# Optimization experiments

Measured on AMD Instinct MI355X. Metric: run time of the kernel, lower is better.

The kernel has to match this reference:

```python
import jax, jax.numpy as jnp
import numpy as np

N = 100000      # nodes
E = 1600000     # edges
IN = 128        # in_channels
ED = 32         # edge_dim
H = 4           # heads
C = 32          # out_channels per head
NEG_SLOPE = 0.2


def setup_inputs() -> dict:
    key = jax.random.key(0)
    ks = jax.random.split(key, 10)
    s = 0.1  # glorot-ish scale
    return {
        "x": jax.random.normal(ks[0], (N, IN), dtype=jnp.float32),
        "edge_index": jax.random.randint(ks[1], (2, E), 0, N, dtype=jnp.int32),
        "edge_attr": jax.random.normal(ks[2], (E, ED), dtype=jnp.float32),
        "W": jax.random.normal(ks[3], (IN, H * C), dtype=jnp.float32) * s,
        "att_src": jax.random.normal(ks[4], (H, C), dtype=jnp.float32) * s,
        "att_dst": jax.random.normal(ks[5], (H, C), dtype=jnp.float32) * s,
        "W_edge": jax.random.normal(ks[6], (ED, H * C), dtype=jnp.float32) * s,
        "att_edge": jax.random.normal(ks[7], (H, C), dtype=jnp.float32) * s,
        "gat_bias": jnp.zeros((H * C,), dtype=jnp.float32),
        "bias": jnp.zeros((C,), dtype=jnp.float32),
    }


def reference(x, edge_index, edge_attr, W, att_src, att_dst, W_edge, att_edge, gat_bias, bias):
    # eval mode: no dropout. GATConv with edge_dim, concat=True, then mean over heads.
    src, dst = edge_index[0], edge_index[1]
    xh = (x @ W).reshape(N, H, C)                       # [N,H,C]
    a_src = jnp.einsum("nhc,hc->nh", xh, att_src)      # [N,H]
    a_dst = jnp.einsum("nhc,hc->nh", xh, att_dst)      # [N,H]
    eh = (edge_attr @ W_edge).reshape(E, H, C)          # [E,H,C]
    a_edge = jnp.einsum("ehc,hc->eh", eh, att_edge)    # [E,H]
    logits = a_src[src] + a_dst[dst] + a_edge           # [E,H]
    logits = jnp.where(logits >= 0, logits, NEG_SLOPE * logits)  # leaky_relu
    # segment softmax over edges grouped by destination node
    seg_max = jax.ops.segment_max(logits, dst, num_segments=N)  # [N,H]
    expv = jnp.exp(logits - seg_max[dst])
    denom = jax.ops.segment_sum(expv, dst, num_segments=N)      # [N,H]
    alpha = expv / denom[dst]                                    # [E,H]
    msg = xh[src] * alpha[:, :, None]                            # [E,H,C]
    out = jax.ops.segment_sum(msg, dst, num_segments=N)          # [N,H,C]
    out = out + gat_bias.reshape(1, H, C)                        # GATConv bias (concat)
    out = out.mean(axis=1)                                       # combine='mean' -> [N,C]
    out = out + bias
    return jax.nn.relu(out)
```

## Files before the change

### kernel.cpp

```cpp
#include <hip/hip_runtime.h>
#include <hip/hip_bf16.h>

typedef __hip_bfloat16 bf16;

#define N_NODES 100000
#define N_EDGES 1600000
#define IN_CH   128
#define ED_DIM  32
#define HEADS   4
#define C_OUT   32
#define HC      128
#define NEG_SLOPE 0.2f
#define SCAN_BLOCKS 98
#define BP_SLICES 8
#define BP_SLICE_N 12500
#define BP_CHUNKS 6250
#define PREP_BLOCKS 392

__device__ __forceinline__ float bf_lo(unsigned u) { return __uint_as_float(u << 16); }
__device__ __forceinline__ float bf_hi(unsigned u) { return __uint_as_float(u & 0xffff0000u); }
__device__ __forceinline__ unsigned short f2bf_rne(float f) {
    unsigned u = __float_as_uint(f);
    return (unsigned short)((u + 0x7fffu + ((u >> 16) & 1u)) >> 16);
}
__device__ __forceinline__ unsigned pack_bf2(float a, float b) {
    return ((unsigned)f2bf_rne(b) << 16) | f2bf_rne(a);
}
__device__ __forceinline__ float load_any(const void* p, int i, int isf32) {
    return isf32 ? ((const float*)p)[i]
                 : __uint_as_float(((unsigned)((const unsigned short*)p)[i]) << 16);
}

__global__ void report_err(unsigned short* out, float code) {
    if (threadIdx.x < 16) out[threadIdx.x] = f2bf_rne(code);
}

__global__ __launch_bounds__(256) void prep_small(
    const void* __restrict__ x,
    const void* __restrict__ W, const void* __restrict__ att_src,
    const void* __restrict__ att_dst, const void* __restrict__ W_edge,
    const void* __restrict__ att_edge, const void* __restrict__ gat_bias,
    const void* __restrict__ bias,
    int* __restrict__ flag,
    unsigned short* __restrict__ Wc, float* __restrict__ att_src_f,
    float* __restrict__ att_dst_f, float* __restrict__ gat_bias_f,
    float* __restrict__ bias_f, float* __restrict__ Wa,
    int* __restrict__ count) {

    int t = threadIdx.x;
    int gi = blockIdx.x * 256 + t;
    if (gi < N_NODES) count[gi] = 0;
    if (blockIdx.x != 0) return;

    __shared__ int cnt;
    if (t == 0) cnt = 0;
    __syncthreads();
    unsigned xw = ((const unsigned*)x)[t];
    int ex = (xw >> 7) & 0xFF;
    if (ex >= 140) atomicAdd(&cnt, 1);
    __syncthreads();
    int isf32 = (cnt >= 32) ? 1 : 0;
    if (t == 0) *flag = isf32;

    for (int i = t; i < IN_CH * HC; i += 256)
        Wc[i] = f2bf_rne(load_any(W, i, isf32));
    if (t < 128) {
        att_src_f[t]  = load_any(att_src, t, isf32);
        att_dst_f[t]  = load_any(att_dst, t, isf32);
        gat_bias_f[t] = load_any(gat_bias, t, isf32);
    }
    if (t < 32) bias_f[t] = load_any(bias, t, isf32);
    if (t < 128) {
        int d = t & 31, h = t >> 5;
        float acc = 0.f;
        for (int c = 0; c < C_OUT; ++c)
            acc += load_any(W_edge, d * HC + h * C_OUT + c, isf32) *
                   load_any(att_edge, h * C_OUT + c, isf32);
        Wa[h * 32 + d] = acc;
    }
}

__global__ __launch_bounds__(256) void node_gemm(
    const int* __restrict__ flag, const void* __restrict__ x,
    const unsigned short* __restrict__ Wc,
    const float* __restrict__ att_src_f, const float* __restrict__ att_dst_f,
    unsigned short* __restrict__ xh,
    float* __restrict__ a_src, float* __restrict__ a_dst) {

    __shared__ unsigned short Wl[IN_CH * HC];
    __shared__ float xl[32 * IN_CH];

    int isf32 = *flag;
    int t = threadIdx.x;
    int node0 = blockIdx.x * 32;

    const uint4* Wg = (const uint4*)Wc;
    uint4* Wl4 = (uint4*)Wl;
#pragma unroll
    for (int k = 0; k < 8; ++k) Wl4[t + k * 256] = Wg[t + k * 256];

    if (isf32) {
        const float4* xg = (const float4*)((const float*)x + (size_t)node0 * IN_CH);
        float4* xl4 = (float4*)xl;
#pragma unroll
        for (int k = 0; k < 4; ++k) xl4[t + k * 256] = xg[t + k * 256];
    } else {
        const unsigned* xg = (const unsigned*)((const unsigned short*)x + (size_t)node0 * IN_CH);
#pragma unroll
        for (int k = 0; k < 8; ++k) {
            unsigned u = xg[t + k * 256];
            int f = 2 * (t + k * 256);
            xl[f]     = bf_lo(u);
            xl[f + 1] = bf_hi(u);
        }
    }
    __syncthreads();

    int q  = t & 31;
    int i0 = (t >> 5) * 4;
    int j4 = q * 4;
    float acc[16];
#pragma unroll
    for (int k = 0; k < 16; ++k) acc[k] = 0.f;

    const float* xr0 = xl + (i0 + 0) * IN_CH;
    const float* xr1 = xl + (i0 + 1) * IN_CH;
    const float* xr2 = xl + (i0 + 2) * IN_CH;
    const float* xr3 = xl + (i0 + 3) * IN_CH;

#pragma unroll 8
    for (int d = 0; d < IN_CH; ++d) {
        uint2 wb = *(const uint2*)(Wl + d * HC + j4);
        float w0 = bf_lo(wb.x), w1 = bf_hi(wb.x);
        float w2 = bf_lo(wb.y), w3 = bf_hi(wb.y);
        float x0 = xr0[d], x1 = xr1[d], x2 = xr2[d], x3 = xr3[d];
        acc[0]  += x0 * w0; acc[1]  += x0 * w1; acc[2]  += x0 * w2; acc[3]  += x0 * w3;
        acc[4]  += x1 * w0; acc[5]  += x1 * w1; acc[6]  += x1 * w2; acc[7]  += x1 * w3;
        acc[8]  += x2 * w0; acc[9]  += x2 * w1; acc[10] += x2 * w2; acc[11] += x2 * w3;
        acc[12] += x3 * w0; acc[13] += x3 * w1; acc[14] += x3 * w2; acc[15] += x3 * w3;
    }

    float4 sa = *(const float4*)(att_src_f + j4);
    float4 da = *(const float4*)(att_dst_f + j4);

#pragma unroll
    for (int k = 0; k < 4; ++k) {
        int node = node0 + i0 + k;
        float a0 = acc[4 * k], a1 = acc[4 * k + 1], a2 = acc[4 * k + 2], a3 = acc[4 * k + 3];
        *(uint2*)(xh + (size_t)node * HC + j4) =
            make_uint2(pack_bf2(a0, a1), pack_bf2(a2, a3));

        float ps = a0 * sa.x + a1 * sa.y + a2 * sa.z + a3 * sa.w;
        float pd = a0 * da.x + a1 * da.y + a2 * da.z + a3 * da.w;
        ps += __shfl_xor(ps, 1); ps += __shfl_xor(ps, 2); ps += __shfl_xor(ps, 4);
        pd += __shfl_xor(pd, 1); pd += __shfl_xor(pd, 2); pd += __shfl_xor(pd, 4);
        if ((q & 7) == 0) {
            int h = q >> 3;
            a_src[node * HEADS + h] = ps;
            a_dst[node * HEADS + h] = pd;
        }
    }
}

__global__ __launch_bounds__(256) void edge_w(
    const int* __restrict__ flag,
    const int* __restrict__ ei, const void* __restrict__ edge_attr,
    const float* __restrict__ a_src, const float* __restrict__ a_dst,
    const float* __restrict__ Wa,
    uint2* __restrict__ w4b, int* __restrict__ count) {

    __shared__ float WaL[128];
    int t = threadIdx.x;
    if (t < 128) WaL[t] = Wa[t];
    __syncthreads();

    int isf32 = *flag;
    int e = blockIdx.x * 256 + t;
    if (e >= N_EDGES) return;
    int s  = ei[e];
    int dn = ei[N_EDGES + e];

    atomicAdd(&count[dn], 1);

    float ae0 = 0.f, ae1 = 0.f, ae2 = 0.f, ae3 = 0.f;
    if (isf32) {
        const float4* ea = (const float4*)((const float*)edge_attr + (size_t)e * ED_DIM);
#pragma unroll
        for (int k = 0; k < 8; ++k) {
            float4 v = ea[k];
            int d = 4 * k;
            ae0 += v.x * WaL[d] + v.y * WaL[d + 1] + v.z * WaL[d + 2] + v.w * WaL[d + 3];
            ae1 += v.x * WaL[32 + d] + v.y * WaL[33 + d] + v.z * WaL[34 + d] + v.w * WaL[35 + d];
            ae2 += v.x * WaL[64 + d] + v.y * WaL[65 + d] + v.z * WaL[66 + d] + v.w * WaL[67 + d];
            ae3 += v.x * WaL[96 + d] + v.y * WaL[97 + d] + v.z * WaL[98 + d] + v.w * WaL[99 + d];
        }
    } else {
        const uint4* ea = (const uint4*)((const unsigned short*)edge_attr + (size_t)e * ED_DIM);
#pragma unroll
        for (int k = 0; k < 4; ++k) {
            uint4 v = ea[k];
            float g0 = bf_lo(v.x), g1 = bf_hi(v.x), g2 = bf_lo(v.y), g3 = bf_hi(v.y);
            float g4 = bf_lo(v.z), g5 = bf_hi(v.z), g6 = bf_lo(v.w), g7 = bf_hi(v.w);
            int d = 8 * k;
            ae0 += g0*WaL[d] + g1*WaL[d+1] + g2*WaL[d+2] + g3*WaL[d+3]
                 + g4*WaL[d+4] + g5*WaL[d+5] + g6*WaL[d+6] + g7*WaL[d+7];
            ae1 += g0*WaL[32+d] + g1*WaL[33+d] + g2*WaL[34+d] + g3*WaL[35+d]
                 + g4*WaL[36+d] + g5*WaL[37+d] + g6*WaL[38+d] + g7*WaL[39+d];
            ae2 += g0*WaL[64+d] + g1*WaL[65+d] + g2*WaL[66+d] + g3*WaL[67+d]
                 + g4*WaL[68+d] + g5*WaL[69+d] + g6*WaL[70+d] + g7*WaL[71+d];
            ae3 += g0*WaL[96+d] + g1*WaL[97+d] + g2*WaL[98+d] + g3*WaL[99+d]
                 + g4*WaL[100+d] + g5*WaL[101+d] + g6*WaL[102+d] + g7*WaL[103+d];
        }
    }

    float4 as = *(const float4*)(a_src + (size_t)s * 4);
    float4 ad = *(const float4*)(a_dst + (size_t)dn * 4);
    float l0 = as.x + ad.x + ae0;
    float l1 = as.y + ad.y + ae1;
    float l2 = as.z + ad.z + ae2;
    float l3 = as.w + ad.w + ae3;
    l0 = (l0 >= 0.f) ? l0 : NEG_SLOPE * l0;
    l1 = (l1 >= 0.f) ? l1 : NEG_SLOPE * l1;
    l2 = (l2 >= 0.f) ? l2 : NEG_SLOPE * l2;
    l3 = (l3 >= 0.f) ? l3 : NEG_SLOPE * l3;
    float w0 = __expf(l0), w1 = __expf(l1), w2 = __expf(l2), w3 = __expf(l3);

    w4b[e] = make_uint2(pack_bf2(w0, w1), pack_bf2(w2, w3));
}

__global__ __launch_bounds__(256) void scan_a(const int* __restrict__ count,
                                              int* __restrict__ starts,
                                              int* __restrict__ blockSums) {
    __shared__ int sd[256];
    int t = threadIdx.x;
    int base = blockIdx.x * 1024 + t * 4;
    int c0 = (base + 0 < N_NODES) ? count[base + 0] : 0;
    int c1 = (base + 1 < N_NODES) ? count[base + 1] : 0;
    int c2 = (base + 2 < N_NODES) ? count[base + 2] : 0;
    int c3 = (base + 3 < N_NODES) ? count[base + 3] : 0;
    int s = c0 + c1 + c2 + c3;
    sd[t] = s;
    __syncthreads();
    for (int off = 1; off < 256; off <<= 1) {
        int v = (t >= off) ? sd[t - off] : 0;
        __syncthreads();
        sd[t] += v;
        __syncthreads();
    }
    int excl = sd[t] - s;
    if (base + 0 < N_NODES) starts[base + 0] = excl;
    if (base + 1 < N_NODES) starts[base + 1] = excl + c0;
    if (base + 2 < N_NODES) starts[base + 2] = excl + c0 + c1;
    if (base + 3 < N_NODES) starts[base + 3] = excl + c0 + c1 + c2;
    if (t == 255) blockSums[blockIdx.x] = sd[255];
}

__global__ __launch_bounds__(128) void scan_b(int* __restrict__ blockSums) {
    __shared__ int sd[128];
    int t = threadIdx.x;
    int v = (t < SCAN_BLOCKS) ? blockSums[t] : 0;
    sd[t] = v;
    __syncthreads();
    for (int off = 1; off < 128; off <<= 1) {
        int u = (t >= off) ? sd[t - off] : 0;
        __syncthreads();
        sd[t] += u;
        __syncthreads();
    }
    if (t < SCAN_BLOCKS) blockSums[t] = sd[t] - v;
}

__global__ __launch_bounds__(256) void scan_c(int* __restrict__ starts,
                                              int* __restrict__ cursor,
                                              const int* __restrict__ blockSums) {
    int off = blockSums[blockIdx.x];
    int base = blockIdx.x * 1024 + threadIdx.x * 4;
#pragma unroll
    for (int k = 0; k < 4; ++k) {
        int idx = base + k;
        if (idx < N_NODES) {
            int v = starts[idx] + off;
            starts[idx] = v;
            cursor[idx] = v;
        }
    }
    if (blockIdx.x == 0 && threadIdx.x == 0) starts[N_NODES] = N_EDGES;
}

__global__ __launch_bounds__(256) void build_perm(
    const int* __restrict__ ei, const uint2* __restrict__ w4b,
    int* __restrict__ cursor, uint4* __restrict__ perm4) {
    int slice = blockIdx.x & 7;
    int e = (blockIdx.x >> 3) * 256 + threadIdx.x;
    if (e >= N_EDGES) return;
    int dn = ei[N_EDGES + e];
    if (dn < slice * BP_SLICE_N || dn >= (slice + 1) * BP_SLICE_N) return;
    int s = ei[e];
    uint2 wv = w4b[e];
    int pos = atomicAdd(&cursor[dn], 1);
    perm4[pos] = make_uint4((unsigned)s, wv.x, wv.y, 0u);
}

__global__ __launch_bounds__(256) void gather(
    const int* __restrict__ flag,
    const int* __restrict__ starts, const uint4* __restrict__ perm4,
    const unsigned short* __restrict__ xh,
    const float* __restrict__ gat_bias_f, const float* __restrict__ bias_f,
    void* __restrict__ out) {

    __shared__ uint4 sR[4][64];

    int t = threadIdx.x;
    int w = t >> 6, lane = t & 63;
    int quarter = lane >> 4;
    int l = lane & 15;
    int h = l >> 2;
    int n = blockIdx.x * 4 + w;
    if (n >= N_NODES) return;
    int isf32 = *flag;

    int st = starts[n], en = starts[n + 1];
    float f0 = 0.f, f1 = 0.f, f2 = 0.f, f3 = 0.f;
    float f4 = 0.f, f5 = 0.f, f6 = 0.f, f7 = 0.f, wsum = 0.f;

    for (int base = st; base < en; base += 64) {
        int cnt = en - base;
        if (cnt > 64) cnt = 64;
        __builtin_amdgcn_wave_barrier();
        if (lane < cnt) sR[w][lane] = perm4[base + lane];
        __builtin_amdgcn_wave_barrier();
#pragma unroll 4
        for (int jj = 0; jj < cnt; jj += 4) {
            int j = jj + quarter;
            int valid = (j < cnt);
            int jc = valid ? j : jj;
            uint4 r = sR[w][jc];
            int s = (int)r.x;
            unsigned hw = (h & 2) ? r.z : r.y;
            float wt = (h & 1) ? bf_hi(hw) : bf_lo(hw);
            wt = valid ? wt : 0.f;
            uint4 xv = *(const uint4*)(xh + ((size_t)s << 7) + 8 * l);
            f0 += wt * bf_lo(xv.x);
            f1 += wt * bf_hi(xv.x);
            f2 += wt * bf_lo(xv.y);
            f3 += wt * bf_hi(xv.y);
            f4 += wt * bf_lo(xv.z);
            f5 += wt * bf_hi(xv.z);
            f6 += wt * bf_lo(xv.w);
            f7 += wt * bf_hi(xv.w);
            wsum += wt;
        }
    }

    f0 += __shfl_xor(f0, 16); f0 += __shfl_xor(f0, 32);
    f1 += __shfl_xor(f1, 16); f1 += __shfl_xor(f1, 32);
    f2 += __shfl_xor(f2, 16); f2 += __shfl_xor(f2, 32);
    f3 += __shfl_xor(f3, 16); f3 += __shfl_xor(f3, 32);
    f4 += __shfl_xor(f4, 16); f4 += __shfl_xor(f4, 32);
    f5 += __shfl_xor(f5, 16); f5 += __shfl_xor(f5, 32);
    f6 += __shfl_xor(f6, 16); f6 += __shfl_xor(f6, 32);
    f7 += __shfl_xor(f7, 16); f7 += __shfl_xor(f7, 32);
    wsum += __shfl_xor(wsum, 16); wsum += __shfl_xor(wsum, 32);

    float inv = (wsum > 0.f) ? 1.f / wsum : 0.f;
    int cg = 8 * l;
    float v0 = f0 * inv + gat_bias_f[cg];
    float v1 = f1 * inv + gat_bias_f[cg + 1];
    float v2 = f2 * inv + gat_bias_f[cg + 2];
    float v3 = f3 * inv + gat_bias_f[cg + 3];
    float v4 = f4 * inv + gat_bias_f[cg + 4];
    float v5 = f5 * inv + gat_bias_f[cg + 5];
    float v6 = f6 * inv + gat_bias_f[cg + 6];
    float v7 = f7 * inv + gat_bias_f[cg + 7];
    v0 += __shfl_xor(v0, 4); v0 += __shfl_xor(v0, 8);
    v1 += __shfl_xor(v1, 4); v1 += __shfl_xor(v1, 8);
    v2 += __shfl_xor(v2, 4); v2 += __shfl_xor(v2, 8);
    v3 += __shfl_xor(v3, 4); v3 += __shfl_xor(v3, 8);
    v4 += __shfl_xor(v4, 4); v4 += __shfl_xor(v4, 8);
    v5 += __shfl_xor(v5, 4); v5 += __shfl_xor(v5, 8);
    v6 += __shfl_xor(v6, 4); v6 += __shfl_xor(v6, 8);
    v7 += __shfl_xor(v7, 4); v7 += __shfl_xor(v7, 8);

    if (lane < 4) {
        int c = 8 * lane;
        float o0 = fmaxf(v0 * 0.25f + bias_f[c],     0.f);
        float o1 = fmaxf(v1 * 0.25f + bias_f[c + 1], 0.f);
        float o2 = fmaxf(v2 * 0.25f + bias_f[c + 2], 0.f);
        float o3 = fmaxf(v3 * 0.25f + bias_f[c + 3], 0.f);
        float o4 = fmaxf(v4 * 0.25f + bias_f[c + 4], 0.f);
        float o5 = fmaxf(v5 * 0.25f + bias_f[c + 5], 0.f);
        float o6 = fmaxf(v6 * 0.25f + bias_f[c + 6], 0.f);
        float o7 = fmaxf(v7 * 0.25f + bias_f[c + 7], 0.f);
        if (isf32) {
            float* op = (float*)out + (size_t)n * C_OUT + c;
            *(float4*)(op)     = make_float4(o0, o1, o2, o3);
            *(float4*)(op + 4) = make_float4(o4, o5, o6, o7);
        } else {
            unsigned p0 = ((unsigned)f2bf_rne(o1) << 16) | f2bf_rne(o0);
            unsigned p1 = ((unsigned)f2bf_rne(o3) << 16) | f2bf_rne(o2);
            unsigned p2 = ((unsigned)f2bf_rne(o5) << 16) | f2bf_rne(o4);
            unsigned p3 = ((unsigned)f2bf_rne(o7) << 16) | f2bf_rne(o6);
            *(uint4*)((unsigned short*)out + (size_t)n * C_OUT + c) =
                make_uint4(p0, p1, p2, p3);
        }
    }
}

extern "C" void kernel_launch(void* const* d_in, const int* in_sizes, int n_in,
                              void* d_out, int out_size, void* d_ws, size_t ws_size,
                              hipStream_t stream) {
    const void* x         = d_in[0];
    const int*  ei        = (const int*)d_in[1];
    const void* edge_attr = d_in[2];
    const void* W         = d_in[3];
    const void* att_src   = d_in[4];
    const void* att_dst   = d_in[5];
    const void* W_edge    = d_in[6];
    const void* att_edge  = d_in[7];
    const void* gat_bias  = d_in[8];
    const void* bias      = d_in[9];

    char* ws = (char*)d_ws;
    size_t off = 0;
    auto align256 = [](size_t v) { return (v + 255) & ~(size_t)255; };

    unsigned short* xh = (unsigned short*)(ws + off);
    off = align256(off + (size_t)N_NODES * HC * sizeof(unsigned short));
    float* a_src_w = (float*)(ws + off);
    off = align256(off + (size_t)N_NODES * HEADS * sizeof(float));
    float* a_dst_w = (float*)(ws + off);
    off = align256(off + (size_t)N_NODES * HEADS * sizeof(float));
    int* count = (int*)(ws + off);
    off = align256(off + (size_t)N_NODES * sizeof(int));
    int* starts = (int*)(ws + off);
    off = align256(off + (size_t)(N_NODES + 1) * sizeof(int));
    int* cursor = (int*)(ws + off);
    off = align256(off + (size_t)N_NODES * sizeof(int));
    int* blockSums = (int*)(ws + off);
    off = align256(off + (size_t)SCAN_BLOCKS * sizeof(int));
    uint2* w4b = (uint2*)(ws + off);
    off = align256(off + (size_t)N_EDGES * sizeof(uint2));
    uint4* perm4 = (uint4*)(ws + off);
    off = align256(off + (size_t)N_EDGES * sizeof(uint4));
    float* Wa = (float*)(ws + off);
    off = align256(off + 128 * sizeof(float));
    unsigned short* Wc = (unsigned short*)(ws + off);
    off = align256(off + (size_t)IN_CH * HC * sizeof(unsigned short));
    float* att_src_f = (float*)(ws + off);
    off = align256(off + 128 * sizeof(float));
    float* att_dst_f = (float*)(ws + off);
    off = align256(off + 128 * sizeof(float));
    float* gat_bias_f = (float*)(ws + off);
    off = align256(off + 128 * sizeof(float));
    float* bias_f = (float*)(ws + off);
    off = align256(off + 32 * sizeof(float));
    int* dflag = (int*)(ws + off);
    off = align256(off + sizeof(int));
    size_t need = off;

    if (ws_size < need) {
        report_err<<<1, 64, 0, stream>>>((unsigned short*)d_out, 1500.0f);
        return;
    }

    (void)hipGetLastError();

    prep_small<<<PREP_BLOCKS, 256, 0, stream>>>(x, W, att_src, att_dst,
                                                W_edge, att_edge, gat_bias, bias,
                                                dflag, Wc, att_src_f, att_dst_f,
                                                gat_bias_f, bias_f, Wa, count);
    node_gemm<<<N_NODES / 32, 256, 0, stream>>>(dflag, x, Wc, att_src_f,
                                                att_dst_f, xh, a_src_w, a_dst_w);
    edge_w<<<(N_EDGES + 255) / 256, 256, 0, stream>>>(dflag, ei, edge_attr,
                                                      a_src_w, a_dst_w, Wa,
                                                      w4b, count);
    scan_a<<<SCAN_BLOCKS, 256, 0, stream>>>(count, starts, blockSums);
    scan_b<<<1, 128, 0, stream>>>(blockSums);
    scan_c<<<SCAN_BLOCKS, 256, 0, stream>>>(starts, cursor, blockSums);
    build_perm<<<BP_SLICES * BP_CHUNKS, 256, 0, stream>>>(ei, w4b, cursor, perm4);
    gather<<<N_NODES / 4, 256, 0, stream>>>(dflag, starts, perm4,
                                            xh, gat_bias_f, bias_f, d_out);

    hipError_t e = hipGetLastError();
    if (e != hipSuccess) {
        report_err<<<1, 64, 0, stream>>>((unsigned short*)d_out,
                                         1000.0f + (float)(int)e);
    }
}
```

Baseline: 574.8 us.

## Fuse degree counting into node GEMM and edge weights into CSR scatter

Measured after the change: 650.3 us. +13.1%, slower.

```diff
diff --git a/kernel.cpp b/kernel.cpp
--- a/kernel.cpp
+++ b/kernel.cpp
@@ -16,6 +16,7 @@
 #define BP_SLICE_N 12500
 #define BP_CHUNKS 6250
 #define PREP_BLOCKS 392
+#define NG_BLOCKS 3125
 
 __device__ __forceinline__ float bf_lo(unsigned u) { return __uint_as_float(u << 16); }
 __device__ __forceinline__ float bf_hi(unsigned u) { return __uint_as_float(u & 0xffff0000u); }
@@ -82,10 +83,12 @@
 
 __global__ __launch_bounds__(256) void node_gemm(
     const int* __restrict__ flag, const void* __restrict__ x,
+    const int* __restrict__ ei,
     const unsigned short* __restrict__ Wc,
     const float* __restrict__ att_src_f, const float* __restrict__ att_dst_f,
     unsigned short* __restrict__ xh,
-    float* __restrict__ a_src, float* __restrict__ a_dst) {
+    float* __restrict__ a_src, float* __restrict__ a_dst,
+    int* __restrict__ count) {
 
     __shared__ unsigned short Wl[IN_CH * HC];
     __shared__ float xl[32 * IN_CH];
@@ -93,6 +96,13 @@
     int isf32 = *flag;
     int t = threadIdx.x;
     int node0 = blockIdx.x * 32;
+
+    {
+        const uint2* dst2 = (const uint2*)(ei + N_EDGES);
+        uint2 d2 = dst2[blockIdx.x * 256 + t];
+        atomicAdd(&count[d2.x], 1);
+        atomicAdd(&count[d2.y], 1);
+    }
 
     const uint4* Wg = (const uint4*)Wc;
     uint4* Wl4 = (uint4*)Wl;
@@ -162,25 +172,84 @@
     }
 }
 
-__global__ __launch_bounds__(256) void edge_w(
+__global__ __launch_bounds__(256) void scan_a(const int* __restrict__ count,
+                                              int* __restrict__ starts,
+                                              int* __restrict__ blockSums) {
+    __shared__ int sd[256];
+    int t = threadIdx.x;
+    int base = blockIdx.x * 1024 + t * 4;
+    int c0 = (base + 0 < N_NODES) ? count[base + 0] : 0;
+    int c1 = (base + 1 < N_NODES) ? count[base + 1] : 0;
+    int c2 = (base + 2 < N_NODES) ? count[base + 2] : 0;
+    int c3 = (base + 3 < N_NODES) ? count[base + 3] : 0;
+    int s = c0 + c1 + c2 + c3;
+    sd[t] = s;
+    __syncthreads();
+    for (int off = 1; off < 256; off <<= 1) {
+        int v = (t >= off) ? sd[t - off] : 0;
+        __syncthreads();
+        sd[t] += v;
+        __syncthreads();
+    }
+    int excl = sd[t] - s;
+    if (base + 0 < N_NODES) starts[base + 0] = excl;
+    if (base + 1 < N_NODES) starts[base + 1] = excl + c0;
+    if (base + 2 < N_NODES) starts[base + 2] = excl + c0 + c1;
+    if (base + 3 < N_NODES) starts[base + 3] = excl + c0 + c1 + c2;
+    if (t == 255) blockSums[blockIdx.x] = sd[255];
+}
+
+__global__ __launch_bounds__(128) void scan_b(int* __restrict__ blockSums) {
+    __shared__ int sd[128];
+    int t = threadIdx.x;
+    int v = (t < SCAN_BLOCKS) ? blockSums[t] : 0;
+    sd[t] = v;
+    __syncthreads();
+    for (int off = 1; off < 128; off <<= 1) {
+        int u = (t >= off) ? sd[t - off] : 0;
+        __syncthreads();
+        sd[t] += u;
+        __syncthreads();
+    }
+    if (t < SCAN_BLOCKS) blockSums[t] = sd[t] - v;
+}
+
+__global__ __launch_bounds__(256) void scan_c(int* __restrict__ starts,
+                                              int* __restrict__ cursor,
+                                              const int* __restrict__ blockSums) {
+    int off = blockSums[blockIdx.x];
+    int base = blockIdx.x * 1024 + threadIdx.x * 4;
+#pragma unroll
+    for (int k = 0; k < 4; ++k) {
+        int idx = base + k;
+        if (idx < N_NODES) {
+            int v = starts[idx] + off;
+            starts[idx] = v;
+            cursor[idx] = v;
+        }
+    }
+    if (blockIdx.x == 0 && threadIdx.x == 0) starts[N_NODES] = N_EDGES;
+}
+
+__global__ __launch_bounds__(256) void edge_scatter(
     const int* __restrict__ flag,
     const int* __restrict__ ei, const void* __restrict__ edge_attr,
     const float* __restrict__ a_src, const float* __restrict__ a_dst,
     const float* __restrict__ Wa,
-    uint2* __restrict__ w4b, int* __restrict__ count) {
+    int* __restrict__ cursor, uint4* __restrict__ perm4) {
 
     __shared__ float WaL[128];
     int t = threadIdx.x;
     if (t < 128) WaL[t] = Wa[t];
     __syncthreads();
 
+    int slice = blockIdx.x & 7;
+    int e = (blockIdx.x >> 3) * 256 + t;
+    if (e >= N_EDGES) return;
+    int dn = ei[N_EDGES + e];
+    if (dn < slice * BP_SLICE_N || dn >= (slice + 1) * BP_SLICE_N) return;
+    int s = ei[e];
     int isf32 = *flag;
-    int e = blockIdx.x * 256 + t;
-    if (e >= N_EDGES) return;
-    int s  = ei[e];
-    int dn = ei[N_EDGES + e];
-
-    atomicAdd(&count[dn], 1);
 
     float ae0 = 0.f, ae1 = 0.f, ae2 = 0.f, ae3 = 0.f;
     if (isf32) {
@@ -225,80 +294,8 @@
     l3 = (l3 >= 0.f) ? l3 : NEG_SLOPE * l3;
     float w0 = __expf(l0), w1 = __expf(l1), w2 = __expf(l2), w3 = __expf(l3);
 
-    w4b[e] = make_uint2(pack_bf2(w0, w1), pack_bf2(w2, w3));
-}
-
-__global__ __launch_bounds__(256) void scan_a(const int* __restrict__ count,
-                                              int* __restrict__ starts,
-                                              int* __restrict__ blockSums) {
-    __shared__ int sd[256];
-    int t = threadIdx.x;
-    int base = blockIdx.x * 1024 + t * 4;
-    int c0 = (base + 0 < N_NODES) ? count[base + 0] : 0;
-    int c1 = (base + 1 < N_NODES) ? count[base + 1] : 0;
-    int c2 = (base + 2 < N_NODES) ? count[base + 2] : 0;
-    int c3 = (base + 3 < N_NODES) ? count[base + 3] : 0;
-    int s = c0 + c1 + c2 + c3;
-    sd[t] = s;
-    __syncthreads();
-    for (int off = 1; off < 256; off <<= 1) {
-        int v = (t >= off) ? sd[t - off] : 0;
-        __syncthreads();
-        sd[t] += v;
-        __syncthreads();
-    }
-    int excl = sd[t] - s;
-    if (base + 0 < N_NODES) starts[base + 0] = excl;
-    if (base + 1 < N_NODES) starts[base + 1] = excl + c0;
-    if (base + 2 < N_NODES) starts[base + 2] = excl + c0 + c1;
-    if (base + 3 < N_NODES) starts[base + 3] = excl + c0 + c1 + c2;
-    if (t == 255) blockSums[blockIdx.x] = sd[255];
-}
-
-__global__ __launch_bounds__(128) void scan_b(int* __restrict__ blockSums) {
-    __shared__ int sd[128];
-    int t = threadIdx.x;
-    int v = (t < SCAN_BLOCKS) ? blockSums[t] : 0;
-    sd[t] = v;
-    __syncthreads();
-    for (int off = 1; off < 128; off <<= 1) {
-        int u = (t >= off) ? sd[t - off] : 0;
-        __syncthreads();
-        sd[t] += u;
-        __syncthreads();
-    }
-    if (t < SCAN_BLOCKS) blockSums[t] = sd[t] - v;
-}
-
-__global__ __launch_bounds__(256) void scan_c(int* __restrict__ starts,
-                                              int* __restrict__ cursor,
-                                              const int* __restrict__ blockSums) {
-    int off = blockSums[blockIdx.x];
-    int base = blockIdx.x * 1024 + threadIdx.x * 4;
-#pragma unroll
-    for (int k = 0; k < 4; ++k) {
-        int idx = base + k;
-        if (idx < N_NODES) {
-            int v = starts[idx] + off;
-            starts[idx] = v;
-            cursor[idx] = v;
-        }
-    }
-    if (blockIdx.x == 0 && threadIdx.x == 0) starts[N_NODES] = N_EDGES;
-}
-
-__global__ __launch_bounds__(256) void build_perm(
-    const int* __restrict__ ei, const uint2* __restrict__ w4b,
-    int* __restrict__ cursor, uint4* __restrict__ perm4) {
-    int slice = blockIdx.x & 7;
-    int e = (blockIdx.x >> 3) * 256 + threadIdx.x;
-    if (e >= N_EDGES) return;
-    int dn = ei[N_EDGES + e];
-    if (dn < slice * BP_SLICE_N || dn >= (slice + 1) * BP_SLICE_N) return;
-    int s = ei[e];
-    uint2 wv = w4b[e];
     int pos = atomicAdd(&cursor[dn], 1);
-    perm4[pos] = make_uint4((unsigned)s, wv.x, wv.y, 0u);
+    perm4[pos] = make_uint4((unsigned)s, pack_bf2(w0, w1), pack_bf2(w2, w3), 0u);
 }
 
 __global__ __launch_bounds__(256) void gather(
@@ -438,8 +435,6 @@
     off = align256(off + (size_t)N_NODES * sizeof(int));
     int* blockSums = (int*)(ws + off);
     off = align256(off + (size_t)SCAN_BLOCKS * sizeof(int));
-    uint2* w4b = (uint2*)(ws + off);
-    off = align256(off + (size_t)N_EDGES * sizeof(uint2));
     uint4* perm4 = (uint4*)(ws + off);
     off = align256(off + (size_t)N_EDGES * sizeof(uint4));
     float* Wa = (float*)(ws + off);
@@ -469,15 +464,15 @@
                                                 W_edge, att_edge, gat_bias, bias,
                                                 dflag, Wc, att_src_f, att_dst_f,
                                                 gat_bias_f, bias_f, Wa, count);
-    node_gemm<<<N_NODES / 32, 256, 0, stream>>>(dflag, x, Wc, att_src_f,
-                                                att_dst_f, xh, a_src_w, a_dst_w);
-    edge_w<<<(N_EDGES + 255) / 256, 256, 0, stream>>>(dflag, ei, edge_attr,
-                                                      a_src_w, a_dst_w, Wa,
-                                                      w4b, count);
+    node_gemm<<<NG_BLOCKS, 256, 0, stream>>>(dflag, x, ei, Wc, att_src_f,
+                                             att_dst_f, xh, a_src_w, a_dst_w,
+                                             count);
     scan_a<<<SCAN_BLOCKS, 256, 0, stream>>>(count, starts, blockSums);
     scan_b<<<1, 128, 0, stream>>>(blockSums);
     scan_c<<<SCAN_BLOCKS, 256, 0, stream>>>(starts, cursor, blockSums);
-    build_perm<<<BP_SLICES * BP_CHUNKS, 256, 0, stream>>>(ei, w4b, cursor, perm4);
+    edge_scatter<<<BP_SLICES * BP_CHUNKS, 256, 0, stream>>>(dflag, ei, edge_attr,
+                                                            a_src_w, a_dst_w, Wa,
+                                                            cursor, perm4);
     gather<<<N_NODES / 4, 256, 0, stream>>>(dflag, starts, perm4,
                                             xh, gat_bias_f, bias_f, d_out);
 
```
